# Performance work log

Measured on AMD Instinct MI355X. Metric: run time of the kernel, lower is better.

## Reference

```python
import jax, jax.numpy as jnp
import numpy as np
import math

FACTOR = 5


def setup_inputs() -> dict:
    key = jax.random.key(0)
    kq, kk, kv, ki = jax.random.split(key, 4)
    B, L, H, D = 4, 2048, 8, 64
    sample_k = min(FACTOR * int(np.ceil(np.log(L))), L)  # 40
    queries = jax.random.normal(kq, (B, L, H, D), jnp.float32)
    keys = jax.random.normal(kk, (B, L, H, D), jnp.float32)
    values = jax.random.normal(kv, (B, L, H, D), jnp.float32)
    # torch.randint(L_K, (L_Q, sample_k)) in _prob_QK, passed explicitly for determinism
    index_sample = jax.random.randint(ki, (L, sample_k), 0, L, dtype=jnp.int32)
    attn_mask = jnp.zeros((1,), jnp.bool_)  # unused when mask_flag=False
    return {"queries": queries, "keys": keys, "values": values,
            "attn_mask": attn_mask, "index_sample": index_sample}


def reference(queries, keys, values, attn_mask, index_sample):
    # queries/keys/values: [B, L, H, D] -> [B, H, L, D]
    B, L_Q, H, D = queries.shape
    L_K = keys.shape[1]
    Q = jnp.swapaxes(queries, 1, 2)
    K = jnp.swapaxes(keys, 1, 2)
    V = jnp.swapaxes(values, 1, 2)

    n_top = min(FACTOR * int(math.ceil(math.log(L_Q))), L_Q)

    # --- _prob_QK ---
    # K_sample: gather sampled keys per query position -> [B, H, L_Q, sample_k, D]
    K_sample = K[:, :, index_sample, :]
    # Q_K_sample: [B, H, L_Q, sample_k]
    Q_K_sample = jnp.einsum('bhld,bhlsd->bhls', Q, K_sample)
    # sparsity measure M: max - mean(sum/L_K) -> [B, H, L_Q]
    M = Q_K_sample.max(axis=-1) - Q_K_sample.sum(axis=-1) / L_K
    _, M_top = jax.lax.top_k(M, n_top)  # [B, H, n_top]
    # Q_reduce: [B, H, n_top, D]
    Q_reduce = jnp.take_along_axis(Q, M_top[..., None], axis=2)
    # scores over ALL keys for the top queries: [B, H, n_top, L_K]
    scores_top = jnp.einsum('bhud,bhkd->bhuk', Q_reduce, K)

    scale = 1.0 / math.sqrt(D)
    scores_top = scores_top * scale

    # --- _get_initial_context (mask_flag=False): mean of V broadcast over L_Q ---
    context = jnp.broadcast_to(V.mean(axis=2, keepdims=True), (B, H, L_Q, D))

    # --- _update_context: softmax over keys, attend, scatter into context ---
    attn = jax.nn.softmax(scores_top, axis=-1)
    out_sel = jnp.einsum('bhuk,bhkd->bhud', attn, V)  # [B, H, n_top, D]
    bidx = jnp.arange(B)[:, None, None]
    hidx = jnp.arange(H)[None, :, None]
    context = context.at[bidx, hidx, M_top].set(out_sel)
    return context  # [B, H, L_Q, D]
```

## Files before the change

### kernel.cpp

```cpp
#include <hip/hip_runtime.h>
#include <hip/hip_bf16.h>

constexpr int B = 4, L = 2048, H = 8, D = 64, S = 40, TOP = 40;
constexpr int NMB = B * H * L / 4;

__global__ __launch_bounds__(256) void kA(const float* __restrict__ Q, const float* __restrict__ K,
                                          const float* __restrict__ V, const int* __restrict__ idx,
                                          float* __restrict__ M, float* __restrict__ Vpart) {
    __shared__ float4 red[256];
    const int t = threadIdx.x;
    if (blockIdx.x < NMB) {
        int n = blockIdx.x;
        int xcd = n & 7, slot = n >> 3;
        int bh = xcd * 4 + (slot & 3);
        int lb = slot >> 2;
        int lane = t & 63;
        int sq = lane >> 4, dq = lane & 15;
        int b = bh >> 3, h = bh & 7;
        int l = lb * 4 + (t >> 6);
        const float4 q4 = *(const float4*)&Q[(((b * L + l) * H + h) << 6) + dq * 4];
        int myidx = (lane < S) ? idx[l * S + lane] : 0;
        int ki[10];
        #pragma unroll
        for (int i = 0; i < 10; ++i) ki[i] = __shfl(myidx, i * 4 + sq, 64);
        float4 kv[10];
        #pragma unroll
        for (int i = 0; i < 10; ++i)
            kv[i] = *(const float4*)&K[(((b * L + ki[i]) * H + h) << 6) + dq * 4];
        float maxv = -3.4e38f, sumv = 0.f;
        #pragma unroll
        for (int i = 0; i < 10; ++i) {
            float p = q4.x * kv[i].x + q4.y * kv[i].y + q4.z * kv[i].z + q4.w * kv[i].w;
            p += __shfl_xor(p, 1); p += __shfl_xor(p, 2);
            p += __shfl_xor(p, 4); p += __shfl_xor(p, 8);
            maxv = fmaxf(maxv, p); sumv += p;
        }
        maxv = fmaxf(maxv, __shfl_xor(maxv, 16));
        maxv = fmaxf(maxv, __shfl_xor(maxv, 32));
        sumv += __shfl_xor(sumv, 16);
        sumv += __shfl_xor(sumv, 32);
        if (lane == 0) M[bh * L + l] = maxv - sumv * (1.0f / (float)L);
    } else {
        int m = blockIdx.x - NMB;
        int xcd = m & 7, slot = m >> 3;
        int bh = xcd * 4 + (slot & 3);
        int chunk = slot >> 2;
        int b = bh >> 3, h = bh & 7;
        int d4 = t & 15, rr = t >> 4;
        int l0 = chunk * 128;
        float4 acc = make_float4(0.f, 0.f, 0.f, 0.f);
        #pragma unroll
        for (int s = 0; s < 8; ++s) {
            int l = l0 + rr + s * 16;
            float4 v = *(const float4*)&V[(((b * L + l) * H + h) << 6) + d4 * 4];
            acc.x += v.x; acc.y += v.y; acc.z += v.z; acc.w += v.w;
        }
        red[t] = acc;
        __syncthreads();
        #pragma unroll
        for (int off = 8; off > 0; off >>= 1) {
            if (rr < off) {
                float4 o = red[t + off * 16];
                red[t].x += o.x; red[t].y += o.y; red[t].z += o.z; red[t].w += o.w;
            }
            __syncthreads();
        }
        if (rr == 0) *(float4*)&Vpart[(bh * 16 + chunk) * 64 + d4 * 4] = red[t];
    }
}

__global__ __launch_bounds__(256) void kB(const float* __restrict__ M, const float* __restrict__ Vpart,
                                          int* __restrict__ Mtop, float* __restrict__ mean) {
    const int t = threadIdx.x;
    if (blockIdx.x < 32) {
        const int bh = blockIdx.x;
        const int lane = t & 63, wid = t >> 6;
        float v[8];
        #pragma unroll
        for (int j = 0; j < 8; ++j) v[j] = M[bh * L + j * 256 + t];
        float bv = v[0]; int bj = 0;
        #pragma unroll
        for (int j = 1; j < 8; ++j) if (v[j] > bv) { bv = v[j]; bj = j; }
        __shared__ float swv[4];
        __shared__ int   swi[4];
        __shared__ int   winS;
        for (int it = 0; it < TOP; ++it) {
            float cv = bv; int ci = bj * 256 + t;
            #pragma unroll
            for (int m = 1; m < 64; m <<= 1) {
                float ov = __shfl_xor(cv, m); int oi = __shfl_xor(ci, m);
                if (ov > cv || (ov == cv && oi < ci)) { cv = ov; ci = oi; }
            }
            if (lane == 0) { swv[wid] = cv; swi[wid] = ci; }
            __syncthreads();
            if (t == 0) {
                float fv = swv[0]; int fi = swi[0];
                #pragma unroll
                for (int w = 1; w < 4; ++w)
                    if (swv[w] > fv || (swv[w] == fv && swi[w] < fi)) { fv = swv[w]; fi = swi[w]; }
                Mtop[bh * TOP + it] = fi;
                winS = fi;
            }
            __syncthreads();
            const int wl = winS;
            if ((wl & 255) == t) {
                if ((wl >> 8) == 0) v[0] = -3.4e38f;
                if ((wl >> 8) == 1) v[1] = -3.4e38f;
                if ((wl >> 8) == 2) v[2] = -3.4e38f;
                if ((wl >> 8) == 3) v[3] = -3.4e38f;
                if ((wl >> 8) == 4) v[4] = -3.4e38f;
                if ((wl >> 8) == 5) v[5] = -3.4e38f;
                if ((wl >> 8) == 6) v[6] = -3.4e38f;
                if ((wl >> 8) == 7) v[7] = -3.4e38f;
                bv = v[0]; bj = 0;
                #pragma unroll
                for (int j = 1; j < 8; ++j) if (v[j] > bv) { bv = v[j]; bj = j; }
            }
        }
    } else {
        int bh = (blockIdx.x - 32) * 4 + (t >> 6);
        int d = t & 63;
        float s = 0.f;
        #pragma unroll
        for (int c = 0; c < 16; ++c) s += Vpart[(bh * 16 + c) * 64 + d];
        mean[bh * 64 + d] = s * (1.0f / (float)L);
    }
}

template <int CC>
__global__ __launch_bounds__(256, 4) void kC(const float* __restrict__ Q, const float* __restrict__ K,
                                             const float* __restrict__ V, const int* __restrict__ Mtop,
                                             const float* __restrict__ mean, float* __restrict__ Npart,
                                             float* __restrict__ Zpart, float* __restrict__ out) {
    constexpr int NCC = L / CC;
    constexpr int KPT = CC / 32;
    constexpr int LDK = CC + (KPT == 4 ? 4 : 2);
    constexpr int LDP = LDK;
    constexpr int LDV = 68;
    constexpr int KVSZ = (CC * LDV > 64 * LDK) ? CC * LDV : 64 * LDK;
    constexpr int VPT = CC * 16 / 256;
    __shared__ float KV[KVSZ];
    __shared__ float Qs[TOP * 64];
    __shared__ float Ps[TOP * LDP];
    const int t = threadIdx.x;
    const int nsel = B * H * NCC;
    if (blockIdx.x >= nsel) {
        const int N4 = B * H * L * D / 4;
        const float4* m4 = (const float4*)mean;
        float4* o4 = (float4*)out;
        for (int i = (blockIdx.x - nsel) * 256 + t; i < N4; i += 2048 * 256) {
            int bh = i >> 15, d4 = i & 15;
            o4[i] = m4[bh * 16 + d4];
        }
        return;
    }
    const int bh = blockIdx.x / NCC, kc = blockIdx.x % NCC;
    const int b = bh >> 3, h = bh & 7;
    const int k0 = kc * CC;
    for (int i = t; i < CC * 16; i += 256) {
        int kk = i >> 4, d4 = i & 15;
        float4 kv = *(const float4*)&K[(((b * L + k0 + kk) * H + h) << 6) + d4 * 4];
        KV[(d4 * 4 + 0) * LDK + kk] = kv.x;
        KV[(d4 * 4 + 1) * LDK + kk] = kv.y;
        KV[(d4 * 4 + 2) * LDK + kk] = kv.z;
        KV[(d4 * 4 + 3) * LDK + kk] = kv.w;
    }
    for (int i = t; i < TOP * 16; i += 256) {
        int u = i >> 4, d4 = i & 15;
        int lsel = Mtop[bh * TOP + u];
        *(float4*)&Qs[u * 64 + d4 * 4] =
            *(const float4*)&Q[(((b * L + lsel) * H + h) << 6) + d4 * 4];
    }
    float4 vpre[VPT];
    #pragma unroll
    for (int p = 0; p < VPT; ++p) {
        int i = p * 256 + t;
        int kk = i >> 4, d4 = i & 15;
        vpre[p] = *(const float4*)&V[(((b * L + k0 + kk) * H + h) << 6) + d4 * 4];
    }
    __syncthreads();
    const int k2 = t & 31, ug = t >> 5;
    float acc[5][KPT];
    #pragma unroll
    for (int j = 0; j < 5; ++j)
        #pragma unroll
        for (int p = 0; p < KPT; ++p) acc[j][p] = 0.f;
    #pragma unroll 4
    for (int d4 = 0; d4 < 16; ++d4) {
        float kr[4][KPT];
        #pragma unroll
        for (int rr = 0; rr < 4; ++rr)
            #pragma unroll
            for (int p = 0; p < KPT; ++p)
                kr[rr][p] = KV[(d4 * 4 + rr) * LDK + k2 * KPT + p];
        #pragma unroll
        for (int j = 0; j < 5; ++j) {
            float4 q4 = *(const float4*)&Qs[(ug * 5 + j) * 64 + d4 * 4];
            #pragma unroll
            for (int p = 0; p < KPT; ++p)
                acc[j][p] += q4.x * kr[0][p] + q4.y * kr[1][p] + q4.z * kr[2][p] + q4.w * kr[3][p];
        }
    }
    #pragma unroll
    for (int j = 0; j < 5; ++j) {
        int u = ug * 5 + j;
        float z = 0.f;
        #pragma unroll
        for (int p = 0; p < KPT; ++p) {
            float e = __expf(acc[j][p] * 0.125f - 16.0f);
            Ps[u * LDP + k2 * KPT + p] = e;
            z += e;
        }
        z += __shfl_xor(z, 1); z += __shfl_xor(z, 2); z += __shfl_xor(z, 4);
        z += __shfl_xor(z, 8); z += __shfl_xor(z, 16);
        if (k2 == 0) Zpart[(bh * TOP + u) * NCC + kc] = z;
    }
    __syncthreads();
    #pragma unroll
    for (int p = 0; p < VPT; ++p) {
        int i = p * 256 + t;
        int kk = i >> 4, d4 = i & 15;
        *(float4*)&KV[kk * LDV + d4 * 4] = vpre[p];
    }
    __syncthreads();
    const int d4v = t & 15, ug2 = t >> 4;
    float4 o0 = make_float4(0,0,0,0), o1 = make_float4(0,0,0,0), o2 = make_float4(0,0,0,0);
    #pragma unroll 4
    for (int kk = 0; kk < CC; ++kk) {
        float4 vv = *(const float4*)&KV[kk * LDV + d4v * 4];
        float e0 = Ps[ug2 * LDP + kk];
        float e1 = Ps[(ug2 + 16) * LDP + kk];
        o0.x += e0 * vv.x; o0.y += e0 * vv.y; o0.z += e0 * vv.z; o0.w += e0 * vv.w;
        o1.x += e1 * vv.x; o1.y += e1 * vv.y; o1.z += e1 * vv.z; o1.w += e1 * vv.w;
        if (ug2 < 8) {
            float e2 = Ps[(ug2 + 32) * LDP + kk];
            o2.x += e2 * vv.x; o2.y += e2 * vv.y; o2.z += e2 * vv.z; o2.w += e2 * vv.w;
        }
    }
    *(float4*)&Npart[((bh * TOP + ug2) * NCC + kc) * 64 + d4v * 4] = o0;
    *(float4*)&Npart[((bh * TOP + ug2 + 16) * NCC + kc) * 64 + d4v * 4] = o1;
    if (ug2 < 8)
        *(float4*)&Npart[((bh * TOP + ug2 + 32) * NCC + kc) * 64 + d4v * 4] = o2;
}

template <int NCC>
__global__ __launch_bounds__(256) void kD(const int* __restrict__ Mtop, const float* __restrict__ Npart,
                                          const float* __restrict__ Zpart, float* __restrict__ out) {
    const int t = threadIdx.x;
    const int g = blockIdx.x * 4 + (t >> 6);
    const int d = t & 63;
    const int bh = g / TOP;
    const int lsel = Mtop[g];
    float z = 0.f;
    #pragma unroll
    for (int c = 0; c < NCC; ++c) z += Zpart[g * NCC + c];
    float n = 0.f;
    #pragma unroll
    for (int c = 0; c < NCC; ++c) n += Npart[(g * NCC + c) * 64 + d];
    out[((bh * L + lsel) << 6) + d] = n / z;
}

__global__ void fill_ctx(const float* __restrict__ mean, float4* __restrict__ out) {
    const int N4 = B * H * L * D / 4;
    for (int i = blockIdx.x * 256 + threadIdx.x; i < N4; i += gridDim.x * 256) {
        int bh = i >> 15, d4 = i & 15;
        out[i] = ((const float4*)mean)[bh * 16 + d4];
    }
}
__global__ void sel_attn(const float* __restrict__ Q, const float* __restrict__ K,
                         const float* __restrict__ V, const int* __restrict__ Mtop,
                         float* __restrict__ out) {
    __shared__ float qs[D];
    __shared__ float p[L];
    __shared__ float red[256];
    int blk = blockIdx.x;
    int bh = blk / TOP, u = blk - bh * TOP;
    int b = bh >> 3, h = bh & 7;
    int t = threadIdx.x;
    int lsel = Mtop[bh * TOP + u];
    if (t < 64) qs[t] = Q[(((b * L + lsel) * H + h) << 6) + t];
    __syncthreads();
    float lsum = 0.f;
    for (int kk = 0; kk < 8; ++kk) {
        int k = kk * 256 + t;
        const float4* krow = (const float4*)&K[((b * L + k) * H + h) << 6];
        const float4* q4 = (const float4*)qs;
        float acc = 0.f;
        #pragma unroll
        for (int j = 0; j < 16; ++j) {
            float4 kv = krow[j]; float4 qv = q4[j];
            acc += qv.x * kv.x + qv.y * kv.y + qv.z * kv.z + qv.w * kv.w;
        }
        float e = __expf(acc * 0.125f - 16.0f);
        p[k] = e;
        lsum += e;
    }
    red[t] = lsum; __syncthreads();
    for (int off = 128; off > 0; off >>= 1) {
        if (t < off) red[t] += red[t + off];
        __syncthreads();
    }
    float inv = 1.0f / red[0];
    __syncthreads();
    int d = t & 63, c = t >> 6;
    float acc = 0.f;
    for (int k = c * 512; k < (c + 1) * 512; ++k)
        acc += p[k] * V[(((b * L + k) * H + h) << 6) + d];
    red[t] = acc; __syncthreads();
    if (t < 128) red[t] += red[t + 128];
    __syncthreads();
    if (t < 64) out[((bh * L + lsel) << 6) + t] = (red[t] + red[t + 64]) * inv;
}

extern "C" void kernel_launch(void* const* d_in, const int* in_sizes, int n_in,
                              void* d_out, int out_size, void* d_ws, size_t ws_size,
                              hipStream_t stream) {
    const float* Q = (const float*)d_in[0];
    const float* K = (const float*)d_in[1];
    const float* V = (const float*)d_in[2];
    const int* idx = (const int*)d_in[4];
    float* out = (float*)d_out;

    char* ws = (char*)d_ws;
    const size_t NPB1 = (size_t)B * H * TOP * 32 * 64 * 4;
    const size_t NPB2 = (size_t)B * H * TOP * 16 * 64 * 4;
    auto layout = [&](size_t npb, size_t& persist) {
        size_t e = 163840 + npb;
        persist = (e > 262144 ? e : 262144);
        return persist + 5120 + 8192 + 131072 + 3072;
    };
    size_t p1, p2, p3;
    size_t need1 = layout(NPB1, p1);
    size_t need2 = layout(NPB2, p2);
    size_t need3 = layout(0, p3);
    int tier = (ws_size >= need1) ? 1 : (ws_size >= need2) ? 2 : (ws_size >= need3) ? 3 : 0;
    size_t persist = (tier == 1) ? p1 : (tier == 2) ? p2 : p3;

    float* M     = (float*)ws;
    float* Zpart = (float*)ws;
    float* Npart = (float*)(ws + 163840);
    int*   Mtop  = (int*)(ws + persist);
    float* mean  = (float*)(ws + persist + 5120);
    float* Vpart = (float*)(ws + persist + 5120 + 8192);

    kA<<<NMB + 512, 256, 0, stream>>>(Q, K, V, idx, M, Vpart);
    kB<<<40, 256, 0, stream>>>(M, Vpart, Mtop, mean);
    if (tier == 1) {
        kC<64><<<B * H * 32 + 2048, 256, 0, stream>>>(Q, K, V, Mtop, mean, Npart, Zpart, out);
        kD<32><<<320, 256, 0, stream>>>(Mtop, Npart, Zpart, out);
    } else if (tier == 2) {
        kC<128><<<B * H * 16 + 2048, 256, 0, stream>>>(Q, K, V, Mtop, mean, Npart, Zpart, out);
        kD<16><<<320, 256, 0, stream>>>(Mtop, Npart, Zpart, out);
    } else {
        fill_ctx<<<2048, 256, 0, stream>>>(mean, (float4*)out);
        sel_attn<<<B * H * TOP, 256, 0, stream>>>(Q, K, V, Mtop, out);
    }
}
```

Measured before the change: 113.3 us.

## Process two queries per wave in kA and move context fill into kB

```diff
diff --git a/kernel.cpp b/kernel.cpp
--- a/kernel.cpp
+++ b/kernel.cpp
@@ -2,11 +2,11 @@
 #include <hip/hip_bf16.h>
 
 constexpr int B = 4, L = 2048, H = 8, D = 64, S = 40, TOP = 40;
-constexpr int NMB = B * H * L / 4;
-
-__global__ __launch_bounds__(256) void kA(const float* __restrict__ Q, const float* __restrict__ K,
-                                          const float* __restrict__ V, const int* __restrict__ idx,
-                                          float* __restrict__ M, float* __restrict__ Vpart) {
+constexpr int NMB = B * H * L / 8;
+
+__global__ __launch_bounds__(256, 3) void kA(const float* __restrict__ Q, const float* __restrict__ K,
+                                             const float* __restrict__ V, const int* __restrict__ idx,
+                                             float* __restrict__ M, float* __restrict__ Vpart) {
     __shared__ float4 red[256];
     const int t = threadIdx.x;
     if (blockIdx.x < NMB) {
@@ -14,32 +14,49 @@
         int xcd = n & 7, slot = n >> 3;
         int bh = xcd * 4 + (slot & 3);
         int lb = slot >> 2;
-        int lane = t & 63;
+        int lane = t & 63, wid = t >> 6;
         int sq = lane >> 4, dq = lane & 15;
         int b = bh >> 3, h = bh & 7;
-        int l = lb * 4 + (t >> 6);
-        const float4 q4 = *(const float4*)&Q[(((b * L + l) * H + h) << 6) + dq * 4];
-        int myidx = (lane < S) ? idx[l * S + lane] : 0;
-        int ki[10];
-        #pragma unroll
-        for (int i = 0; i < 10; ++i) ki[i] = __shfl(myidx, i * 4 + sq, 64);
-        float4 kv[10];
-        #pragma unroll
-        for (int i = 0; i < 10; ++i)
-            kv[i] = *(const float4*)&K[(((b * L + ki[i]) * H + h) << 6) + dq * 4];
-        float maxv = -3.4e38f, sumv = 0.f;
+        int l0 = lb * 8 + wid * 2, l1 = l0 + 1;
+        const float4 qa = *(const float4*)&Q[(((b * L + l0) * H + h) << 6) + dq * 4];
+        const float4 qb = *(const float4*)&Q[(((b * L + l1) * H + h) << 6) + dq * 4];
+        int ia = (lane < S) ? idx[l0 * S + lane] : 0;
+        int ib = (lane < S) ? idx[l1 * S + lane] : 0;
+        int kia[10], kib[10];
+        #pragma unroll
+        for (int i = 0; i < 10; ++i) kia[i] = __shfl(ia, i * 4 + sq, 64);
+        #pragma unroll
+        for (int i = 0; i < 10; ++i) kib[i] = __shfl(ib, i * 4 + sq, 64);
+        const float* kbase = &K[((b * L * H + h) << 6) + dq * 4];
+        float4 kva[10], kvb[10];
+        #pragma unroll
+        for (int i = 0; i < 10; ++i) kva[i] = *(const float4*)(kbase + (size_t)kia[i] * (H * D));
+        #pragma unroll
+        for (int i = 0; i < 10; ++i) kvb[i] = *(const float4*)(kbase + (size_t)kib[i] * (H * D));
+        float mva = -3.4e38f, sva = 0.f;
         #pragma unroll
         for (int i = 0; i < 10; ++i) {
-            float p = q4.x * kv[i].x + q4.y * kv[i].y + q4.z * kv[i].z + q4.w * kv[i].w;
+            float p = qa.x * kva[i].x + qa.y * kva[i].y + qa.z * kva[i].z + qa.w * kva[i].w;
             p += __shfl_xor(p, 1); p += __shfl_xor(p, 2);
             p += __shfl_xor(p, 4); p += __shfl_xor(p, 8);
-            maxv = fmaxf(maxv, p); sumv += p;
-        }
-        maxv = fmaxf(maxv, __shfl_xor(maxv, 16));
-        maxv = fmaxf(maxv, __shfl_xor(maxv, 32));
-        sumv += __shfl_xor(sumv, 16);
-        sumv += __shfl_xor(sumv, 32);
-        if (lane == 0) M[bh * L + l] = maxv - sumv * (1.0f / (float)L);
+            mva = fmaxf(mva, p); sva += p;
+        }
+        float mvb = -3.4e38f, svb = 0.f;
+        #pragma unroll
+        for (int i = 0; i < 10; ++i) {
+            float p = qb.x * kvb[i].x + qb.y * kvb[i].y + qb.z * kvb[i].z + qb.w * kvb[i].w;
+            p += __shfl_xor(p, 1); p += __shfl_xor(p, 2);
+            p += __shfl_xor(p, 4); p += __shfl_xor(p, 8);
+            mvb = fmaxf(mvb, p); svb += p;
+        }
+        mva = fmaxf(mva, __shfl_xor(mva, 16)); mva = fmaxf(mva, __shfl_xor(mva, 32));
+        sva += __shfl_xor(sva, 16); sva += __shfl_xor(sva, 32);
+        mvb = fmaxf(mvb, __shfl_xor(mvb, 16)); mvb = fmaxf(mvb, __shfl_xor(mvb, 32));
+        svb += __shfl_xor(svb, 16); svb += __shfl_xor(svb, 32);
+        if (lane == 0) {
+            M[bh * L + l0] = mva - sva * (1.0f / (float)L);
+            M[bh * L + l1] = mvb - svb * (1.0f / (float)L);
+        }
     } else {
         int m = blockIdx.x - NMB;
         int xcd = m & 7, slot = m >> 3;
@@ -70,7 +87,7 @@
 }
 
 __global__ __launch_bounds__(256) void kB(const float* __restrict__ M, const float* __restrict__ Vpart,
-                                          int* __restrict__ Mtop, float* __restrict__ mean) {
+                                          int* __restrict__ Mtop, float* __restrict__ out) {
     const int t = threadIdx.x;
     if (blockIdx.x < 32) {
         const int bh = blockIdx.x;
@@ -118,20 +135,28 @@
             }
         }
     } else {
-        int bh = (blockIdx.x - 32) * 4 + (t >> 6);
-        int d = t & 63;
-        float s = 0.f;
-        #pragma unroll
-        for (int c = 0; c < 16; ++c) s += Vpart[(bh * 16 + c) * 64 + d];
-        mean[bh * 64 + d] = s * (1.0f / (float)L);
+        __shared__ float smean[64];
+        int f = blockIdx.x - 32;
+        int i0 = f * 512;
+        int bh = i0 >> 15;
+        if (t < 64) {
+            float s = 0.f;
+            #pragma unroll
+            for (int c = 0; c < 16; ++c) s += Vpart[(bh * 16 + c) * 64 + t];
+            smean[t] = s * (1.0f / (float)L);
+        }
+        __syncthreads();
+        const float4* m4 = (const float4*)smean;
+        float4* o4 = (float4*)out;
+        o4[i0 + t]       = m4[t & 15];
+        o4[i0 + 256 + t] = m4[t & 15];
     }
 }
 
 template <int CC>
 __global__ __launch_bounds__(256, 4) void kC(const float* __restrict__ Q, const float* __restrict__ K,
                                              const float* __restrict__ V, const int* __restrict__ Mtop,
-                                             const float* __restrict__ mean, float* __restrict__ Npart,
-                                             float* __restrict__ Zpart, float* __restrict__ out) {
+                                             float* __restrict__ Npart, float* __restrict__ Zpart) {
     constexpr int NCC = L / CC;
     constexpr int KPT = CC / 32;
     constexpr int LDK = CC + (KPT == 4 ? 4 : 2);
@@ -143,17 +168,6 @@
     __shared__ float Qs[TOP * 64];
     __shared__ float Ps[TOP * LDP];
     const int t = threadIdx.x;
-    const int nsel = B * H * NCC;
-    if (blockIdx.x >= nsel) {
-        const int N4 = B * H * L * D / 4;
-        const float4* m4 = (const float4*)mean;
-        float4* o4 = (float4*)out;
-        for (int i = (blockIdx.x - nsel) * 256 + t; i < N4; i += 2048 * 256) {
-            int bh = i >> 15, d4 = i & 15;
-            o4[i] = m4[bh * 16 + d4];
-        }
-        return;
-    }
     const int bh = blockIdx.x / NCC, kc = blockIdx.x % NCC;
     const int b = bh >> 3, h = bh & 7;
     const int k0 = kc * CC;
@@ -260,13 +274,6 @@
     out[((bh * L + lsel) << 6) + d] = n / z;
 }
 
-__global__ void fill_ctx(const float* __restrict__ mean, float4* __restrict__ out) {
-    const int N4 = B * H * L * D / 4;
-    for (int i = blockIdx.x * 256 + threadIdx.x; i < N4; i += gridDim.x * 256) {
-        int bh = i >> 15, d4 = i & 15;
-        out[i] = ((const float4*)mean)[bh * 16 + d4];
-    }
-}
 __global__ void sel_attn(const float* __restrict__ Q, const float* __restrict__ K,
                          const float* __restrict__ V, const int* __restrict__ Mtop,
                          float* __restrict__ out) {
@@ -340,19 +347,17 @@
     float* Zpart = (float*)ws;
     float* Npart = (float*)(ws + 163840);
     int*   Mtop  = (int*)(ws + persist);
-    float* mean  = (float*)(ws + persist + 5120);
     float* Vpart = (float*)(ws + persist + 5120 + 8192);
 
     kA<<<NMB + 512, 256, 0, stream>>>(Q, K, V, idx, M, Vpart);
-    kB<<<40, 256, 0, stream>>>(M, Vpart, Mtop, mean);
+    kB<<<32 + 2048, 256, 0, stream>>>(M, Vpart, Mtop, out);
     if (tier == 1) {
-        kC<64><<<B * H * 32 + 2048, 256, 0, stream>>>(Q, K, V, Mtop, mean, Npart, Zpart, out);
+        kC<64><<<B * H * 32, 256, 0, stream>>>(Q, K, V, Mtop, Npart, Zpart);
         kD<32><<<320, 256, 0, stream>>>(Mtop, Npart, Zpart, out);
     } else if (tier == 2) {
-        kC<128><<<B * H * 16 + 2048, 256, 0, stream>>>(Q, K, V, Mtop, mean, Npart, Zpart, out);
+        kC<128><<<B * H * 16, 256, 0, stream>>>(Q, K, V, Mtop, Npart, Zpart);
         kD<16><<<320, 256, 0, stream>>>(Mtop, Npart, Zpart, out);
     } else {
-        fill_ctx<<<2048, 256, 0, stream>>>(mean, (float4*)out);
         sel_attn<<<B * H * TOP, 256, 0, stream>>>(Q, K, V, Mtop, out);
     }
 }
```

Result: slower. 117.4 us (+3.6%).

## Fuse four-kernel pipeline into one persistent cooperative kernel with grid syncs

Applied to the files above, without the earlier changes.

```diff
diff --git a/kernel.cpp b/kernel.cpp
--- a/kernel.cpp
+++ b/kernel.cpp
@@ -1,12 +1,292 @@
 #include <hip/hip_runtime.h>
 #include <hip/hip_bf16.h>
+#include <hip/hip_cooperative_groups.h>
+
+namespace cg = cooperative_groups;
 
 constexpr int B = 4, L = 2048, H = 8, D = 64, S = 40, TOP = 40;
-constexpr int NMB = B * H * L / 4;
-
-__global__ __launch_bounds__(256) void kA(const float* __restrict__ Q, const float* __restrict__ K,
-                                          const float* __restrict__ V, const int* __restrict__ idx,
-                                          float* __restrict__ M, float* __restrict__ Vpart) {
+constexpr int NMT = B * H * L / 4;
+constexpr int NMB = B * H * L / 8;
+constexpr int CCM = 64, NCCM = L / CCM;
+
+typedef float f32x4 __attribute__((ext_vector_type(4)));
+
+
+__device__ __forceinline__ void bodyM(int task, int t, const float* __restrict__ Q,
+                                      const float* __restrict__ K, const int* __restrict__ idx,
+                                      float* __restrict__ M) {
+    int xcd = task & 7, slot = task >> 3;
+    int bh = xcd * 4 + (slot & 3);
+    int lb = slot >> 2;
+    int lane = t & 63;
+    int sq = lane >> 4, dq = lane & 15;
+    int b = bh >> 3, h = bh & 7;
+    int l = lb * 4 + (t >> 6);
+    const float4 q4 = *(const float4*)&Q[(((b * L + l) * H + h) << 6) + dq * 4];
+    int myidx = (lane < S) ? idx[l * S + lane] : 0;
+    int ki[10];
+    #pragma unroll
+    for (int i = 0; i < 10; ++i) ki[i] = __shfl(myidx, i * 4 + sq, 64);
+    float4 kv[10];
+    #pragma unroll
+    for (int i = 0; i < 10; ++i)
+        kv[i] = *(const float4*)&K[(((b * L + ki[i]) * H + h) << 6) + dq * 4];
+    float maxv = -3.4e38f, sumv = 0.f;
+    #pragma unroll
+    for (int i = 0; i < 10; ++i) {
+        float p = q4.x * kv[i].x + q4.y * kv[i].y + q4.z * kv[i].z + q4.w * kv[i].w;
+        p += __shfl_xor(p, 1); p += __shfl_xor(p, 2);
+        p += __shfl_xor(p, 4); p += __shfl_xor(p, 8);
+        maxv = fmaxf(maxv, p); sumv += p;
+    }
+    maxv = fmaxf(maxv, __shfl_xor(maxv, 16));
+    maxv = fmaxf(maxv, __shfl_xor(maxv, 32));
+    sumv += __shfl_xor(sumv, 16);
+    sumv += __shfl_xor(sumv, 32);
+    if (lane == 0) M[bh * L + l] = maxv - sumv * (1.0f / (float)L);
+}
+
+__device__ __forceinline__ void bodyVmean(int m, int t, const float* __restrict__ V,
+                                          float* __restrict__ Vpart, float* smem) {
+    float4* red = (float4*)smem;
+    int xcd = m & 7, slot = m >> 3;
+    int bh = xcd * 4 + (slot & 3);
+    int chunk = slot >> 2;
+    int b = bh >> 3, h = bh & 7;
+    int d4 = t & 15, rr = t >> 4;
+    int l0 = chunk * 128;
+    float4 acc = make_float4(0.f, 0.f, 0.f, 0.f);
+    #pragma unroll
+    for (int s = 0; s < 8; ++s) {
+        int l = l0 + rr + s * 16;
+        float4 v = *(const float4*)&V[(((b * L + l) * H + h) << 6) + d4 * 4];
+        acc.x += v.x; acc.y += v.y; acc.z += v.z; acc.w += v.w;
+    }
+    __syncthreads();
+    red[t] = acc;
+    __syncthreads();
+    #pragma unroll
+    for (int off = 8; off > 0; off >>= 1) {
+        if (rr < off) {
+            float4 o = red[t + off * 16];
+            red[t].x += o.x; red[t].y += o.y; red[t].z += o.z; red[t].w += o.w;
+        }
+        __syncthreads();
+    }
+    if (rr == 0) *(float4*)&Vpart[(bh * 16 + chunk) * 64 + d4 * 4] = red[t];
+}
+
+__device__ __forceinline__ void bodyTopk(int bh, int t, const float* __restrict__ M,
+                                         int* __restrict__ Mtop, float* smem) {
+    float* swv = smem;
+    int*   swi = (int*)(smem + 4);
+    int*   winS = (int*)(smem + 8);
+    const int lane = t & 63, wid = t >> 6;
+    float v[8];
+    #pragma unroll
+    for (int j = 0; j < 8; ++j) v[j] = M[bh * L + j * 256 + t];
+    float bv = v[0]; int bj = 0;
+    #pragma unroll
+    for (int j = 1; j < 8; ++j) if (v[j] > bv) { bv = v[j]; bj = j; }
+    for (int it = 0; it < TOP; ++it) {
+        float cv = bv; int ci = bj * 256 + t;
+        #pragma unroll
+        for (int m = 1; m < 64; m <<= 1) {
+            float ov = __shfl_xor(cv, m); int oi = __shfl_xor(ci, m);
+            if (ov > cv || (ov == cv && oi < ci)) { cv = ov; ci = oi; }
+        }
+        if (lane == 0) { swv[wid] = cv; swi[wid] = ci; }
+        __syncthreads();
+        if (t == 0) {
+            float fv = swv[0]; int fi = swi[0];
+            #pragma unroll
+            for (int w = 1; w < 4; ++w)
+                if (swv[w] > fv || (swv[w] == fv && swi[w] < fi)) { fv = swv[w]; fi = swi[w]; }
+            Mtop[bh * TOP + it] = fi;
+            *winS = fi;
+        }
+        __syncthreads();
+        const int wl = *winS;
+        if ((wl & 255) == t) {
+            if ((wl >> 8) == 0) v[0] = -3.4e38f;
+            if ((wl >> 8) == 1) v[1] = -3.4e38f;
+            if ((wl >> 8) == 2) v[2] = -3.4e38f;
+            if ((wl >> 8) == 3) v[3] = -3.4e38f;
+            if ((wl >> 8) == 4) v[4] = -3.4e38f;
+            if ((wl >> 8) == 5) v[5] = -3.4e38f;
+            if ((wl >> 8) == 6) v[6] = -3.4e38f;
+            if ((wl >> 8) == 7) v[7] = -3.4e38f;
+            bv = v[0]; bj = 0;
+            #pragma unroll
+            for (int j = 1; j < 8; ++j) if (v[j] > bv) { bv = v[j]; bj = j; }
+        }
+    }
+}
+
+__device__ __forceinline__ void bodyFill(int f, int t, const float* __restrict__ Vpart,
+                                         float* __restrict__ out, float* smem) {
+    float* smean = smem;
+    int i0 = f * 512;
+    int bh = i0 >> 15;
+    __syncthreads();
+    if (t < 64) {
+        float s = 0.f;
+        #pragma unroll
+        for (int c = 0; c < 16; ++c) s += Vpart[(bh * 16 + c) * 64 + t];
+        smean[t] = s * (1.0f / (float)L);
+    }
+    __syncthreads();
+    const float4* m4 = (const float4*)smean;
+    float4* o4 = (float4*)out;
+    o4[i0 + t]       = m4[t & 15];
+    o4[i0 + 256 + t] = m4[t & 15];
+}
+
+__device__ __forceinline__ void bodyKC(int task, int t, const float* __restrict__ Q,
+                                       const float* __restrict__ K, const float* __restrict__ V,
+                                       const int* __restrict__ Mtop, float* __restrict__ Npart,
+                                       float* __restrict__ Zpart, float* smem) {
+    constexpr int CC = CCM, NCC = NCCM;
+    constexpr int KPT = 2, LDK = 66, LDP = 66, LDV = 68, VPT = 4;
+    float* KV = smem;
+    float* Qs = smem + 4352;
+    float* Ps = smem + 6912;
+    const int bh = task / NCC, kc = task % NCC;
+    const int b = bh >> 3, h = bh & 7;
+    const int k0 = kc * CC;
+    __syncthreads();
+    for (int i = t; i < CC * 16; i += 256) {
+        int kk = i >> 4, d4 = i & 15;
+        float4 kv = *(const float4*)&K[(((b * L + k0 + kk) * H + h) << 6) + d4 * 4];
+        KV[(d4 * 4 + 0) * LDK + kk] = kv.x;
+        KV[(d4 * 4 + 1) * LDK + kk] = kv.y;
+        KV[(d4 * 4 + 2) * LDK + kk] = kv.z;
+        KV[(d4 * 4 + 3) * LDK + kk] = kv.w;
+    }
+    for (int i = t; i < TOP * 16; i += 256) {
+        int u = i >> 4, d4 = i & 15;
+        int lsel = Mtop[bh * TOP + u];
+        *(float4*)&Qs[u * 64 + d4 * 4] =
+            *(const float4*)&Q[(((b * L + lsel) * H + h) << 6) + d4 * 4];
+    }
+    float4 vpre[VPT];
+    #pragma unroll
+    for (int p = 0; p < VPT; ++p) {
+        int i = p * 256 + t;
+        int kk = i >> 4, d4 = i & 15;
+        vpre[p] = *(const float4*)&V[(((b * L + k0 + kk) * H + h) << 6) + d4 * 4];
+    }
+    __syncthreads();
+    const int k2 = t & 31, ug = t >> 5;
+    float acc[5][KPT];
+    #pragma unroll
+    for (int j = 0; j < 5; ++j)
+        #pragma unroll
+        for (int p = 0; p < KPT; ++p) acc[j][p] = 0.f;
+    #pragma unroll 4
+    for (int d4 = 0; d4 < 16; ++d4) {
+        float kr[4][KPT];
+        #pragma unroll
+        for (int rr = 0; rr < 4; ++rr)
+            #pragma unroll
+            for (int p = 0; p < KPT; ++p)
+                kr[rr][p] = KV[(d4 * 4 + rr) * LDK + k2 * KPT + p];
+        #pragma unroll
+        for (int j = 0; j < 5; ++j) {
+            float4 q4 = *(const float4*)&Qs[(ug * 5 + j) * 64 + d4 * 4];
+            #pragma unroll
+            for (int p = 0; p < KPT; ++p)
+                acc[j][p] += q4.x * kr[0][p] + q4.y * kr[1][p] + q4.z * kr[2][p] + q4.w * kr[3][p];
+        }
+    }
+    #pragma unroll
+    for (int j = 0; j < 5; ++j) {
+        int u = ug * 5 + j;
+        float z = 0.f;
+        #pragma unroll
+        for (int p = 0; p < KPT; ++p) {
+            float e = __expf(acc[j][p] * 0.125f - 16.0f);
+            Ps[u * LDP + k2 * KPT + p] = e;
+            z += e;
+        }
+        z += __shfl_xor(z, 1); z += __shfl_xor(z, 2); z += __shfl_xor(z, 4);
+        z += __shfl_xor(z, 8); z += __shfl_xor(z, 16);
+        if (k2 == 0) Zpart[(bh * TOP + u) * NCC + kc] = z;
+    }
+    __syncthreads();
+    #pragma unroll
+    for (int p = 0; p < VPT; ++p) {
+        int i = p * 256 + t;
+        int kk = i >> 4, d4 = i & 15;
+        *(float4*)&KV[kk * LDV + d4 * 4] = vpre[p];
+    }
+    __syncthreads();
+    const int d4v = t & 15, ug2 = t >> 4;
+    float4 o0 = make_float4(0,0,0,0), o1 = make_float4(0,0,0,0), o2 = make_float4(0,0,0,0);
+    #pragma unroll 4
+    for (int kk = 0; kk < CC; ++kk) {
+        float4 vv = *(const float4*)&KV[kk * LDV + d4v * 4];
+        float e0 = Ps[ug2 * LDP + kk];
+        float e1 = Ps[(ug2 + 16) * LDP + kk];
+        o0.x += e0 * vv.x; o0.y += e0 * vv.y; o0.z += e0 * vv.z; o0.w += e0 * vv.w;
+        o1.x += e1 * vv.x; o1.y += e1 * vv.y; o1.z += e1 * vv.z; o1.w += e1 * vv.w;
+        if (ug2 < 8) {
+            float e2 = Ps[(ug2 + 32) * LDP + kk];
+            o2.x += e2 * vv.x; o2.y += e2 * vv.y; o2.z += e2 * vv.z; o2.w += e2 * vv.w;
+        }
+    }
+    *(float4*)&Npart[((bh * TOP + ug2) * NCC + kc) * 64 + d4v * 4] = o0;
+    *(float4*)&Npart[((bh * TOP + ug2 + 16) * NCC + kc) * 64 + d4v * 4] = o1;
+    if (ug2 < 8)
+        *(float4*)&Npart[((bh * TOP + ug2 + 32) * NCC + kc) * 64 + d4v * 4] = o2;
+}
+
+__device__ __forceinline__ void bodyKD(int task, int t, const int* __restrict__ Mtop,
+                                       const float* __restrict__ Npart, const float* __restrict__ Zpart,
+                                       float* __restrict__ out) {
+    const int g = task * 4 + (t >> 6);
+    const int d = t & 63;
+    const int bh = g / TOP;
+    const int lsel = Mtop[g];
+    float z = 0.f;
+    #pragma unroll
+    for (int c = 0; c < NCCM; ++c) z += Zpart[g * NCCM + c];
+    float n = 0.f;
+    #pragma unroll
+    for (int c = 0; c < NCCM; ++c) n += Npart[(g * NCCM + c) * 64 + d];
+    out[((bh * L + lsel) << 6) + d] = n / z;
+}
+
+__global__ __launch_bounds__(256, 4) void mega(const float* __restrict__ Q, const float* __restrict__ K,
+                                               const float* __restrict__ V, const int* __restrict__ idx,
+                                               float* __restrict__ out, float* __restrict__ M,
+                                               int* __restrict__ Mtop, float* __restrict__ Vpart,
+                                               float* __restrict__ Npart, float* __restrict__ Zpart) {
+    __shared__ __align__(16) float smem[9552];
+    cg::grid_group grid = cg::this_grid();
+    const int t = threadIdx.x;
+    const int nb = gridDim.x;
+    for (int task = blockIdx.x; task < NMT + 512; task += nb) {
+        if (task < NMT) bodyM(task, t, Q, K, idx, M);
+        else            bodyVmean(task - NMT, t, V, Vpart, smem);
+    }
+    grid.sync();
+    for (int task = blockIdx.x; task < 32 + 2048; task += nb) {
+        if (task < 32) bodyTopk(task, t, M, Mtop, smem);
+        else           bodyFill(task - 32, t, Vpart, out, smem);
+    }
+    grid.sync();
+    for (int task = blockIdx.x; task < B * H * NCCM; task += nb)
+        bodyKC(task, t, Q, K, V, Mtop, Npart, Zpart, smem);
+    grid.sync();
+    for (int task = blockIdx.x; task < 320; task += nb)
+        bodyKD(task, t, Mtop, Npart, Zpart, out);
+}
+
+
+__global__ __launch_bounds__(256, 3) void kA(const float* __restrict__ Q, const float* __restrict__ K,
+                                             const float* __restrict__ V, const int* __restrict__ idx,
+                                             float* __restrict__ M, float* __restrict__ Vpart) {
     __shared__ float4 red[256];
     const int t = threadIdx.x;
     if (blockIdx.x < NMB) {
@@ -14,32 +294,41 @@
         int xcd = n & 7, slot = n >> 3;
         int bh = xcd * 4 + (slot & 3);
         int lb = slot >> 2;
-        int lane = t & 63;
+        int lane = t & 63, wid = t >> 6;
         int sq = lane >> 4, dq = lane & 15;
         int b = bh >> 3, h = bh & 7;
-        int l = lb * 4 + (t >> 6);
-        const float4 q4 = *(const float4*)&Q[(((b * L + l) * H + h) << 6) + dq * 4];
-        int myidx = (lane < S) ? idx[l * S + lane] : 0;
-        int ki[10];
-        #pragma unroll
-        for (int i = 0; i < 10; ++i) ki[i] = __shfl(myidx, i * 4 + sq, 64);
-        float4 kv[10];
-        #pragma unroll
-        for (int i = 0; i < 10; ++i)
-            kv[i] = *(const float4*)&K[(((b * L + ki[i]) * H + h) << 6) + dq * 4];
-        float maxv = -3.4e38f, sumv = 0.f;
+        int l0 = lb * 8 + wid * 2, l1 = l0 + 1;
+        const float4 qa = *(const float4*)&Q[(((b * L + l0) * H + h) << 6) + dq * 4];
+        const float4 qb = *(const float4*)&Q[(((b * L + l1) * H + h) << 6) + dq * 4];
+        int ia = (lane < S) ? idx[l0 * S + lane] : 0;
+        int ib = (lane < S) ? idx[l1 * S + lane] : 0;
+        float mva = -3.4e38f, sva = 0.f, mvb = -3.4e38f, svb = 0.f;
         #pragma unroll
         for (int i = 0; i < 10; ++i) {
-            float p = q4.x * kv[i].x + q4.y * kv[i].y + q4.z * kv[i].z + q4.w * kv[i].w;
+            int kia = __shfl(ia, i * 4 + sq, 64);
+            float4 kv = *(const float4*)&K[(((b * L + kia) * H + h) << 6) + dq * 4];
+            float p = qa.x * kv.x + qa.y * kv.y + qa.z * kv.z + qa.w * kv.w;
             p += __shfl_xor(p, 1); p += __shfl_xor(p, 2);
             p += __shfl_xor(p, 4); p += __shfl_xor(p, 8);
-            maxv = fmaxf(maxv, p); sumv += p;
-        }
-        maxv = fmaxf(maxv, __shfl_xor(maxv, 16));
-        maxv = fmaxf(maxv, __shfl_xor(maxv, 32));
-        sumv += __shfl_xor(sumv, 16);
-        sumv += __shfl_xor(sumv, 32);
-        if (lane == 0) M[bh * L + l] = maxv - sumv * (1.0f / (float)L);
+            mva = fmaxf(mva, p); sva += p;
+        }
+        #pragma unroll
+        for (int i = 0; i < 10; ++i) {
+            int kib = __shfl(ib, i * 4 + sq, 64);
+            float4 kv = *(const float4*)&K[(((b * L + kib) * H + h) << 6) + dq * 4];
+            float p = qb.x * kv.x + qb.y * kv.y + qb.z * kv.z + qb.w * kv.w;
+            p += __shfl_xor(p, 1); p += __shfl_xor(p, 2);
+            p += __shfl_xor(p, 4); p += __shfl_xor(p, 8);
+            mvb = fmaxf(mvb, p); svb += p;
+        }
+        mva = fmaxf(mva, __shfl_xor(mva, 16)); mva = fmaxf(mva, __shfl_xor(mva, 32));
+        sva += __shfl_xor(sva, 16); sva += __shfl_xor(sva, 32);
+        mvb = fmaxf(mvb, __shfl_xor(mvb, 16)); mvb = fmaxf(mvb, __shfl_xor(mvb, 32));
+        svb += __shfl_xor(svb, 16); svb += __shfl_xor(svb, 32);
+        if (lane == 0) {
+            M[bh * L + l0] = mva - sva * (1.0f / (float)L);
+            M[bh * L + l1] = mvb - svb * (1.0f / (float)L);
+        }
     } else {
         int m = blockIdx.x - NMB;
         int xcd = m & 7, slot = m >> 3;
@@ -72,51 +361,9 @@
 __global__ __launch_bounds__(256) void kB(const float* __restrict__ M, const float* __restrict__ Vpart,
                                           int* __restrict__ Mtop, float* __restrict__ mean) {
     const int t = threadIdx.x;
+    __shared__ float smem[16];
     if (blockIdx.x < 32) {
-        const int bh = blockIdx.x;
-        const int lane = t & 63, wid = t >> 6;
-        float v[8];
-        #pragma unroll
-        for (int j = 0; j < 8; ++j) v[j] = M[bh * L + j * 256 + t];
-        float bv = v[0]; int bj = 0;
-        #pragma unroll
-        for (int j = 1; j < 8; ++j) if (v[j] > bv) { bv = v[j]; bj = j; }
-        __shared__ float swv[4];
-        __shared__ int   swi[4];
-        __shared__ int   winS;
-        for (int it = 0; it < TOP; ++it) {
-            float cv = bv; int ci = bj * 256 + t;
-            #pragma unroll
-            for (int m = 1; m < 64; m <<= 1) {
-                float ov = __shfl_xor(cv, m); int oi = __shfl_xor(ci, m);
-                if (ov > cv || (ov == cv && oi < ci)) { cv = ov; ci = oi; }
-            }
-            if (lane == 0) { swv[wid] = cv; swi[wid] = ci; }
-            __syncthreads();
-            if (t == 0) {
-                float fv = swv[0]; int fi = swi[0];
-                #pragma unroll
-                for (int w = 1; w < 4; ++w)
-                    if (swv[w] > fv || (swv[w] == fv && swi[w] < fi)) { fv = swv[w]; fi = swi[w]; }
-                Mtop[bh * TOP + it] = fi;
-                winS = fi;
-            }
-            __syncthreads();
-            const int wl = winS;
-            if ((wl & 255) == t) {
-                if ((wl >> 8) == 0) v[0] = -3.4e38f;
-                if ((wl >> 8) == 1) v[1] = -3.4e38f;
-                if ((wl >> 8) == 2) v[2] = -3.4e38f;
-                if ((wl >> 8) == 3) v[3] = -3.4e38f;
-                if ((wl >> 8) == 4) v[4] = -3.4e38f;
-                if ((wl >> 8) == 5) v[5] = -3.4e38f;
-                if ((wl >> 8) == 6) v[6] = -3.4e38f;
-                if ((wl >> 8) == 7) v[7] = -3.4e38f;
-                bv = v[0]; bj = 0;
-                #pragma unroll
-                for (int j = 1; j < 8; ++j) if (v[j] > bv) { bv = v[j]; bj = j; }
-            }
-        }
+        bodyTopk(blockIdx.x, t, M, Mtop, smem);
     } else {
         int bh = (blockIdx.x - 32) * 4 + (t >> 6);
         int d = t & 63;
@@ -343,12 +590,27 @@
     float* mean  = (float*)(ws + persist + 5120);
     float* Vpart = (float*)(ws + persist + 5120 + 8192);
 
+    if (tier == 1) {
+        int bpc = 0;
+        hipError_t e = hipOccupancyMaxActiveBlocksPerMultiprocessor(&bpc, mega, 256, 0);
+        if (e == hipSuccess && bpc >= 1) {
+            int grid = bpc * 256;
+            if (grid > 4096) grid = 4096;
+            void* params[] = {(void*)&Q, (void*)&K, (void*)&V, (void*)&idx, (void*)&out,
+                              (void*)&M, (void*)&Mtop, (void*)&Vpart, (void*)&Npart, (void*)&Zpart};
+            hipLaunchCooperativeKernel(mega, dim3(grid), dim3(256), params, 0, stream);
+            return;
+        }
+        tier = 2;
+        persist = p2;
+        Mtop  = (int*)(ws + persist);
+        mean  = (float*)(ws + persist + 5120);
+        Vpart = (float*)(ws + persist + 5120 + 8192);
+    }
+
     kA<<<NMB + 512, 256, 0, stream>>>(Q, K, V, idx, M, Vpart);
     kB<<<40, 256, 0, stream>>>(M, Vpart, Mtop, mean);
-    if (tier == 1) {
-        kC<64><<<B * H * 32 + 2048, 256, 0, stream>>>(Q, K, V, Mtop, mean, Npart, Zpart, out);
-        kD<32><<<320, 256, 0, stream>>>(Mtop, Npart, Zpart, out);
-    } else if (tier == 2) {
+    if (tier == 2) {
         kC<128><<<B * H * 16 + 2048, 256, 0, stream>>>(Q, K, V, Mtop, mean, Npart, Zpart, out);
         kD<16><<<320, 256, 0, stream>>>(Mtop, Npart, Zpart, out);
     } else {
```

Measured after the change: 287.7 us. 154% more time.

## Remap sampling kernel to one block per (batch, query) covering all heads

Applied to the files above, without the earlier changes.

```diff
diff --git a/kernel.cpp b/kernel.cpp
--- a/kernel.cpp
+++ b/kernel.cpp
@@ -2,44 +2,57 @@
 #include <hip/hip_bf16.h>
 
 constexpr int B = 4, L = 2048, H = 8, D = 64, S = 40, TOP = 40;
-constexpr int NMB = B * H * L / 4;
-
-__global__ __launch_bounds__(256) void kA(const float* __restrict__ Q, const float* __restrict__ K,
-                                          const float* __restrict__ V, const int* __restrict__ idx,
-                                          float* __restrict__ M, float* __restrict__ Vpart) {
+constexpr int NMB = B * L;
+
+__global__ __launch_bounds__(256, 4) void kA(const float* __restrict__ Q, const float* __restrict__ K,
+                                             const float* __restrict__ V, const int* __restrict__ idx,
+                                             float* __restrict__ M, float* __restrict__ Vpart) {
     __shared__ float4 red[256];
+    __shared__ float wmax[4][8], wsum[4][8];
     const int t = threadIdx.x;
     if (blockIdx.x < NMB) {
         int n = blockIdx.x;
-        int xcd = n & 7, slot = n >> 3;
-        int bh = xcd * 4 + (slot & 3);
-        int lb = slot >> 2;
-        int lane = t & 63;
-        int sq = lane >> 4, dq = lane & 15;
-        int b = bh >> 3, h = bh & 7;
-        int l = lb * 4 + (t >> 6);
-        const float4 q4 = *(const float4*)&Q[(((b * L + l) * H + h) << 6) + dq * 4];
-        int myidx = (lane < S) ? idx[l * S + lane] : 0;
+        int b = n & 3;
+        int l = ((n >> 2) & 1) * 1024 + (n >> 3);
+        int lane = t & 63, w = t >> 6;
+        const float* Qb = Q + ((size_t)(b * L + l) << 9);
+        const float* Kb = K + ((size_t)(b * L) << 9);
+        float4 qa = *(const float4*)(Qb + lane * 4);
+        float4 qb = *(const float4*)(Qb + 256 + lane * 4);
         int ki[10];
         #pragma unroll
-        for (int i = 0; i < 10; ++i) ki[i] = __shfl(myidx, i * 4 + sq, 64);
-        float4 kv[10];
-        #pragma unroll
-        for (int i = 0; i < 10; ++i)
-            kv[i] = *(const float4*)&K[(((b * L + ki[i]) * H + h) << 6) + dq * 4];
-        float maxv = -3.4e38f, sumv = 0.f;
+        for (int i = 0; i < 10; ++i) ki[i] = idx[l * S + w * 10 + i];
+        float4 ka[10], kb[10];
         #pragma unroll
         for (int i = 0; i < 10; ++i) {
-            float p = q4.x * kv[i].x + q4.y * kv[i].y + q4.z * kv[i].z + q4.w * kv[i].w;
-            p += __shfl_xor(p, 1); p += __shfl_xor(p, 2);
-            p += __shfl_xor(p, 4); p += __shfl_xor(p, 8);
-            maxv = fmaxf(maxv, p); sumv += p;
-        }
-        maxv = fmaxf(maxv, __shfl_xor(maxv, 16));
-        maxv = fmaxf(maxv, __shfl_xor(maxv, 32));
-        sumv += __shfl_xor(sumv, 16);
-        sumv += __shfl_xor(sumv, 32);
-        if (lane == 0) M[bh * L + l] = maxv - sumv * (1.0f / (float)L);
+            const float* kr = Kb + ((size_t)ki[i] << 9);
+            ka[i] = *(const float4*)(kr + lane * 4);
+            kb[i] = *(const float4*)(kr + 256 + lane * 4);
+        }
+        float maxa = -3.4e38f, suma = 0.f, maxb = -3.4e38f, sumb = 0.f;
+        #pragma unroll
+        for (int i = 0; i < 10; ++i) {
+            float pa = qa.x * ka[i].x + qa.y * ka[i].y + qa.z * ka[i].z + qa.w * ka[i].w;
+            float pb = qb.x * kb[i].x + qb.y * kb[i].y + qb.z * kb[i].z + qb.w * kb[i].w;
+            pa += __shfl_xor(pa, 1); pa += __shfl_xor(pa, 2);
+            pa += __shfl_xor(pa, 4); pa += __shfl_xor(pa, 8);
+            pb += __shfl_xor(pb, 1); pb += __shfl_xor(pb, 2);
+            pb += __shfl_xor(pb, 4); pb += __shfl_xor(pb, 8);
+            maxa = fmaxf(maxa, pa); suma += pa;
+            maxb = fmaxf(maxb, pb); sumb += pb;
+        }
+        if ((lane & 15) == 0) {
+            int g = lane >> 4;
+            wmax[w][g] = maxa;     wsum[w][g] = suma;
+            wmax[w][g + 4] = maxb; wsum[w][g + 4] = sumb;
+        }
+        __syncthreads();
+        if (t < 8) {
+            float mv = wmax[0][t], sv = wsum[0][t];
+            #pragma unroll
+            for (int ww = 1; ww < 4; ++ww) { mv = fmaxf(mv, wmax[ww][t]); sv += wsum[ww][t]; }
+            M[(b * 8 + t) * L + l] = mv - sv * (1.0f / (float)L);
+        }
     } else {
         int m = blockIdx.x - NMB;
         int xcd = m & 7, slot = m >> 3;
```

New measurement: 109.2 us (median of 2 runs). 3.6% less time.
